# Kernel tuning notes

Hardware: AMD Instinct MI355X
Metric: run time of the kernel (lower is better)

## Reference

```python
import jax, jax.numpy as jnp
import numpy as np

N_NODES, N_EDGES = 8, 8
NODE_FEAT, EDGE_FEAT = 4, 3
NODE_EMB, EDGE_EMB = 9, 8
N_LAYER = 3
N_QUBITS = NODE_EMB + EDGE_EMB + 2  # 19

H_GATE = (jnp.array([[1, 1], [1, -1]], jnp.complex64) / np.sqrt(2).astype(np.float32))
CNOT4 = jnp.asarray(np.array([[1, 0, 0, 0], [0, 1, 0, 0], [0, 0, 0, 1], [0, 0, 1, 0]],
                             np.complex64).reshape(2, 2, 2, 2))


def rx_mat(t):
    c = jnp.cos(0.5 * t).astype(jnp.complex64)
    s = (-1j) * jnp.sin(0.5 * t).astype(jnp.complex64)
    return jnp.stack([jnp.stack([c, s]), jnp.stack([s, c])])


def rz_mat(t):
    e = jnp.exp(-0.5j * t.astype(jnp.complex64))
    z = jnp.zeros((), jnp.complex64)
    return jnp.stack([jnp.stack([e, z]), jnp.stack([z, jnp.conj(e)])])


def apply_1q(psi, U, w):
    psi = jnp.tensordot(U, psi, axes=((1,), (w,)))
    return jnp.moveaxis(psi, 0, w)


def apply_cnot(psi, c, t):
    psi = jnp.tensordot(CNOT4, psi, axes=((2, 3), (c, t)))
    return jnp.moveaxis(psi, (0, 1), (c, t))


def gcn_conv(x, src, dst, W, b, n):
    # PyG GCNConv: add self-loops, symmetric D^-1/2 (A+I) D^-1/2 normalization
    h = x @ W  # (n, out)
    src2 = jnp.concatenate([src, jnp.arange(n)])
    dst2 = jnp.concatenate([dst, jnp.arange(n)])
    deg = jax.ops.segment_sum(jnp.ones(src2.shape[0], x.dtype), dst2, num_segments=n)
    dis = jnp.where(deg > 0, jax.lax.rsqrt(jnp.maximum(deg, 1e-12)), 0.0)
    coef = dis[src2] * dis[dst2]
    out = jax.ops.segment_sum(h[src2] * coef[:, None], dst2, num_segments=n)
    return out + b


def quantum_circuit(feats, qweights):
    psi = jnp.zeros((2,) * N_QUBITS, jnp.complex64).at[(0,) * N_QUBITS].set(1.0)
    # feature_map: Hadamards + BasicEntanglerLayers(1 layer, rotation=RZ)
    for q in range(N_QUBITS):
        psi = apply_1q(psi, H_GATE, q)
    for q in range(N_QUBITS):
        psi = apply_1q(psi, rz_mat(feats[q]), q)
    for q in range(N_QUBITS):
        psi = apply_cnot(psi, q, (q + 1) % N_QUBITS)
    # two ansatz blocks (weights first dim is 2), each with N_LAYER layers
    for i in range(2):
        w = qweights[i]  # (N_QUBITS, N_LAYER)
        for j in range(N_LAYER):
            for q in range(N_QUBITS):
                psi = apply_1q(psi, rx_mat(w[q, j]), q)
                psi = apply_1q(psi, rz_mat(w[q, j]), q)
            for q in range(N_QUBITS):
                psi = apply_cnot(psi, q, (q + 1) % N_QUBITS)
    pr = jnp.sum(jnp.abs(psi.reshape(2, -1)) ** 2, axis=1)  # marginal of qubit 0
    return (pr[0] - pr[1]).astype(jnp.float32)  # <Z_0>


def setup_inputs() -> dict:
    key = jax.random.key(0)
    ks = jax.random.split(key, 20)
    inp = {
        "edge_index": jax.random.randint(ks[0], (2, N_EDGES), 0, N_NODES),
        "state": jax.random.normal(ks[1], (N_NODES, NODE_FEAT), jnp.float32),
        "mass": jax.random.normal(ks[2], (N_EDGES,), jnp.float32),
        "spin": jax.random.normal(ks[3], (N_EDGES,), jnp.float32),
        "charge": jax.random.normal(ks[4], (N_EDGES,), jnp.float32),
        "p_norm": jax.random.normal(ks[5], (1,), jnp.float32),
        "theta": jax.random.normal(ks[6], (1,), jnp.float32),
        "scattering": jax.random.normal(ks[7], (1,), jnp.float32),
        "gcn_node_w": jax.random.normal(ks[8], (NODE_FEAT, 1), jnp.float32) * 0.3,
        "gcn_node_b": jnp.zeros((1,), jnp.float32),
        "gcn_edge_w": jax.random.normal(ks[9], (EDGE_FEAT, 1), jnp.float32) * 0.3,
        "gcn_edge_b": jnp.zeros((1,), jnp.float32),
        "node_w": jax.random.normal(ks[10], (N_NODES, NODE_EMB), jnp.float32) * 0.3,
        "node_b": jnp.zeros((NODE_EMB,), jnp.float32),
        "edge_w": jax.random.normal(ks[11], (N_EDGES, EDGE_EMB), jnp.float32) * 0.3,
        "edge_b": jnp.zeros((EDGE_EMB,), jnp.float32),
        "qweights": jax.random.normal(ks[12], (2, N_QUBITS, N_LAYER), jnp.float32) * 0.1,
    }
    return inp


def reference(edge_index, state, mass, spin, charge, p_norm, theta, scattering,
              gcn_node_w, gcn_node_b, gcn_edge_w, gcn_edge_b,
              node_w, node_b, edge_w, edge_b, qweights):
    src, dst = edge_index[0], edge_index[1]
    x_edges = jnp.stack([mass, spin, charge], axis=1)  # (E, 3)
    x1 = gcn_conv(state, src, dst, gcn_node_w, gcn_node_b, N_NODES).reshape(-1)
    x1 = x1 @ node_w + node_b  # (NODE_EMB,)
    x2 = gcn_conv(x_edges, src, dst, gcn_edge_w, gcn_edge_b, N_EDGES).reshape(-1)
    x2 = x2 @ edge_w + edge_b  # (EDGE_EMB,)
    feats = jnp.concatenate([x1, x2, p_norm.reshape(-1), theta.reshape(-1)])  # (N_QUBITS,)
    return quantum_circuit(feats, qweights)
```

## Files before the change

### kernel.cpp

```cpp
#include <hip/hip_runtime.h>

#define NQ 19
#define SZ (1u << 19)

struct Params {
    const int* ei;
    const float* state; const float* mass; const float* spin; const float* charge;
    const float* p_norm; const float* theta;
    const float* gnw; const float* gnb; const float* gew; const float* geb;
    const float* nw; const float* nb; const float* ew; const float* eb;
    const float* qw;
    float2* buf0;
    unsigned* counter;
};

__device__ __forceinline__ unsigned pinv(unsigned c)
{
    unsigned y = (c ^ (c >> 1)) & 0x1FFFFu;
    unsigned c0 = c & 1u, c17 = (c >> 17) & 1u, c18 = (c >> 18) & 1u;
    return y | ((c0 ^ c17 ^ c18) << 17) | ((c0 ^ c18) << 18);
}

__device__ __forceinline__ unsigned padl(unsigned l) { return l + 2u * (l >> 3); }

__device__ __forceinline__ void bfly(float2& a, float2& b,
                                     float2 u00, float2 u01,
                                     float2 u10, float2 u11)
{
    float2 na, nb;
    na.x = u00.x * a.x - u00.y * a.y + u01.x * b.x - u01.y * b.y;
    na.y = u00.x * a.y + u00.y * a.x + u01.x * b.y + u01.y * b.x;
    nb.x = u10.x * a.x - u10.y * a.y + u11.x * b.x - u11.y * b.y;
    nb.y = u10.x * a.y + u10.y * a.x + u11.x * b.y + u11.y * b.x;
    a = na;
    b = nb;
}

__device__ __forceinline__ void apply_gates(float2 r[4], const float2* Gl,
                                            int ampbit0, int jbit0, int n)
{
    #pragma unroll
    for (int k = 0; k < n; ++k) {
        const float2 u00 = Gl[(ampbit0 + k) * 4 + 0];
        const float2 u01 = Gl[(ampbit0 + k) * 4 + 1];
        const float2 u10 = Gl[(ampbit0 + k) * 4 + 2];
        const float2 u11 = Gl[(ampbit0 + k) * 4 + 3];
        const int m = 1 << (jbit0 + k);
        #pragma unroll
        for (int j = 0; j < 4; ++j)
            if (!(j & m)) bfly(r[j], r[j | m], u00, u01, u10, u11);
    }
}

__device__ __forceinline__ void build_G(float2* shG, const float* qw, int layer,
                                        unsigned t)
{
    if (t < NQ) {
        int k = (int)t, q = 18 - k;
        double th = (double)qw[(layer / 3) * (NQ * 3) + q * 3 + (layer % 3)];
        double c = cos(0.5 * th), s = sin(0.5 * th);
        shG[k * 4 + 0] = make_float2((float)(c * c), (float)(-s * c));
        shG[k * 4 + 1] = make_float2((float)(-s * s), (float)(-c * s));
        shG[k * 4 + 2] = make_float2((float)(s * s), (float)(-c * s));
        shG[k * 4 + 3] = make_float2((float)(c * c), (float)(s * c));
    }
}

__device__ __forceinline__ void passA_tail(float2 r[4], const float2* Gl,
                                           unsigned t, float2* X0, float2* X1)
{
    apply_gates(r, Gl, 0, 0, 2);
    *reinterpret_cast<float4*>(&X0[padl(t << 2)]) =
        make_float4(r[0].x, r[0].y, r[1].x, r[1].y);
    *reinterpret_cast<float4*>(&X0[padl((t << 2) + 2u)]) =
        make_float4(r[2].x, r[2].y, r[3].x, r[3].y);
    __syncthreads();
    #pragma unroll
    for (int j = 0; j < 4; ++j)
        r[j] = X0[padl((t & 3u) | ((unsigned)j << 2) | ((t >> 2) << 4))];
    apply_gates(r, Gl, 2, 0, 2);
    #pragma unroll
    for (int j = 0; j < 4; ++j)
        X1[padl((t & 3u) | ((unsigned)j << 2) | ((t >> 2) << 4))] = r[j];
    __syncthreads();
    #pragma unroll
    for (int j = 0; j < 4; ++j)
        r[j] = X1[padl((t & 15u) | ((unsigned)j << 4) | ((t >> 4) << 6))];
    apply_gates(r, Gl, 4, 0, 2);
    #pragma unroll
    for (int j = 0; j < 4; ++j)
        X0[padl((t & 15u) | ((unsigned)j << 4) | ((t >> 4) << 6))] = r[j];
    __syncthreads();
    #pragma unroll
    for (int j = 0; j < 4; ++j)
        r[j] = X0[padl((t & 63u) | ((unsigned)j << 6) | ((t >> 6) << 8))];
    apply_gates(r, Gl, 6, 0, 2);
    #pragma unroll
    for (int j = 0; j < 4; ++j)
        X1[padl((t & 63u) | ((unsigned)j << 6) | ((t >> 6) << 8))] = r[j];
    __syncthreads();
    #pragma unroll
    for (int j = 0; j < 4; ++j)
        r[j] = X1[padl((t & 255u) | ((unsigned)j << 8) | ((t >> 8) << 10))];
    apply_gates(r, Gl, 8, 0, 2);
    #pragma unroll
    for (int j = 0; j < 4; ++j)
        X0[padl((t & 255u) | ((unsigned)j << 8) | ((t >> 8) << 10))] = r[j];
    __syncthreads();
    #pragma unroll
    for (int j = 0; j < 4; ++j)
        r[j] = X0[padl(t | ((unsigned)j << 9))];
    apply_gates(r, Gl, 10, 1, 1);
}

__device__ __forceinline__ void passB_gates(float2 r[4], const float2* Gl,
                                            unsigned t, float2* X0, float2* X1)
{
    apply_gates(r, Gl, 11, 0, 2);
    #pragma unroll
    for (int j = 0; j < 4; ++j)
        X0[padl((t & 7u) | ((unsigned)j << 3) | ((t >> 3) << 5))] = r[j];
    __syncthreads();
    #pragma unroll
    for (int j = 0; j < 4; ++j)
        r[j] = X0[padl((t & 31u) | ((unsigned)j << 5) | ((t >> 5) << 7))];
    apply_gates(r, Gl, 13, 0, 2);
    #pragma unroll
    for (int j = 0; j < 4; ++j)
        X1[padl((t & 31u) | ((unsigned)j << 5) | ((t >> 5) << 7))] = r[j];
    __syncthreads();
    #pragma unroll
    for (int j = 0; j < 4; ++j)
        r[j] = X1[padl((t & 127u) | ((unsigned)j << 7) | ((t >> 7) << 9))];
    apply_gates(r, Gl, 15, 0, 2);
    #pragma unroll
    for (int j = 0; j < 4; ++j)
        X0[padl((t & 127u) | ((unsigned)j << 7) | ((t >> 7) << 9))] = r[j];
    __syncthreads();
    #pragma unroll
    for (int j = 0; j < 4; ++j)
        r[j] = X0[padl(t | ((unsigned)j << 9))];
    apply_gates(r, Gl, 17, 0, 2);
}

__global__ __launch_bounds__(512, 4)
void k_A0(Params P)
{
    __shared__ __align__(16) float2 stage[5120];
    __shared__ __align__(16) float2 X0[2560];
    __shared__ float2 shG[NQ * 4];
    __shared__ double sh_feats[NQ];
    __shared__ double sh_S;

    const unsigned t = threadIdx.x;
    const unsigned blk = blockIdx.x;
    const unsigned base = blk << 11;

    if (blk == 0 && t == 0) *P.counter = 0u;

    if (t == 0) {
        double deg[8], dis[8], h[8], o1[8], he[8], o2[8];
        for (int v = 0; v < 8; ++v) deg[v] = 1.0;
        for (int e = 0; e < 8; ++e) deg[P.ei[8 + e]] += 1.0;
        for (int v = 0; v < 8; ++v) dis[v] = 1.0 / sqrt(deg[v]);
        for (int v = 0; v < 8; ++v) {
            double s = 0.0;
            for (int k = 0; k < 4; ++k)
                s += (double)P.state[v * 4 + k] * (double)P.gnw[k];
            h[v] = s;
        }
        for (int v = 0; v < 8; ++v) o1[v] = h[v] * dis[v] * dis[v] + (double)P.gnb[0];
        for (int e = 0; e < 8; ++e) {
            int s = P.ei[e], d = P.ei[8 + e];
            o1[d] += h[s] * dis[s] * dis[d];
        }
        for (int j = 0; j < 9; ++j) {
            double a = (double)P.nb[j];
            for (int v = 0; v < 8; ++v) a += o1[v] * (double)P.nw[v * 9 + j];
            sh_feats[j] = a;
        }
        for (int e = 0; e < 8; ++e)
            he[e] = (double)P.mass[e] * (double)P.gew[0]
                  + (double)P.spin[e] * (double)P.gew[1]
                  + (double)P.charge[e] * (double)P.gew[2];
        for (int v = 0; v < 8; ++v) o2[v] = he[v] * dis[v] * dis[v] + (double)P.geb[0];
        for (int e = 0; e < 8; ++e) {
            int s = P.ei[e], d = P.ei[8 + e];
            o2[d] += he[s] * dis[s] * dis[d];
        }
        for (int j = 0; j < 8; ++j) {
            double a = (double)P.eb[j];
            for (int v = 0; v < 8; ++v) a += o2[v] * (double)P.ew[v * 8 + j];
            sh_feats[9 + j] = a;
        }
        sh_feats[17] = (double)P.p_norm[0];
        sh_feats[18] = (double)P.theta[0];
        double S = 0.0;
        for (int q = 0; q < NQ; ++q) S += sh_feats[q];
        sh_S = S;
    }
    __syncthreads();

    build_G(shG, P.qw, 0, t);
    {
        double S = sh_S;
        for (unsigned m = t; m < 1024u; m += 512u) {
            double a = -0.5 * S;
            for (int k = 0; k < 10; ++k)
                if ((m >> k) & 1u) a += sh_feats[18 - k];
            double sp, cp;
            sincos(a, &sp, &cp);
            stage[m] = make_float2((float)cp, (float)sp);
        }
        const double amp = 1.0 / sqrt((double)SZ);
        for (unsigned m = t; m < 512u; m += 512u) {
            double a = 0.0;
            for (int k = 0; k < 9; ++k)
                if ((m >> k) & 1u) a += sh_feats[8 - k];
            double sp, cp;
            sincos(a, &sp, &cp);
            stage[1024u + m] = make_float2((float)(amp * cp), (float)(amp * sp));
        }
    }
    __syncthreads();

    float2 r[4];
    #pragma unroll
    for (int j = 0; j < 4; ++j) {
        unsigned li = (t << 2) | (unsigned)j;
        unsigned b = pinv(base | li);
        float2 e0 = stage[b & 1023u];
        float2 e1 = stage[1024u + (b >> 10)];
        r[j] = make_float2(e0.x * e1.x - e0.y * e1.y,
                           e0.x * e1.y + e0.y * e1.x);
    }
    passA_tail(r, shG, t, X0, stage);
    #pragma unroll
    for (int j = 0; j < 4; ++j)
        P.buf0[base | t | ((unsigned)j << 9)] = r[j];
}

__global__ __launch_bounds__(512, 4)
void k_A(const float2* __restrict__ in, float2* __restrict__ out,
         const float* __restrict__ qw, int layer)
{
    __shared__ __align__(16) float2 stage[5120];
    __shared__ __align__(16) float2 X0[2560];
    __shared__ float2 shG[NQ * 4];
    const unsigned t = threadIdx.x;
    const unsigned base = blockIdx.x << 11;

    build_G(shG, qw, layer, t);
    const unsigned R0 = pinv(base) & ~2047u;
    const unsigned R1 = pinv(base | 1u) & ~2047u;
    #pragma unroll
    for (int k = 0; k < 4; ++k) {
        unsigned i = ((unsigned)k << 10) | (t << 1);
        unsigned g = (i < 2048u) ? (R0 + i) : (R1 + (i - 2048u));
        *reinterpret_cast<float4*>(&stage[padl(i)]) =
            *reinterpret_cast<const float4*>(&in[g]);
    }
    __syncthreads();

    float2 r[4];
    #pragma unroll
    for (int j = 0; j < 4; ++j) {
        unsigned li = (t << 2) | (unsigned)j;
        unsigned b = pinv(base | li);
        r[j] = stage[padl(((li & 1u) << 11) | (b & 2047u))];
    }
    passA_tail(r, shG, t, X0, stage);
    #pragma unroll
    for (int j = 0; j < 4; ++j)
        out[base | t | ((unsigned)j << 9)] = r[j];
}

__global__ __launch_bounds__(512, 4)
void k_B(float2* __restrict__ buf, const float* __restrict__ qw, int layer,
         int do_reduce, double* __restrict__ partial,
         unsigned* __restrict__ counter, float* __restrict__ out)
{
    __shared__ __align__(16) float2 X0[2560];
    __shared__ __align__(16) float2 X1[2560];
    __shared__ double sm[512];
    __shared__ float2 shG[NQ * 4];
    __shared__ int who;
    const unsigned t = threadIdx.x;
    const unsigned blk = blockIdx.x;

    build_G(shG, qw, layer, t);
    float2 r[4];
    #pragma unroll
    for (int j = 0; j < 4; ++j) {
        unsigned li = (t & 7u) | ((unsigned)j << 3) | ((t >> 3) << 5);
        unsigned c = (li & 7u) | (blk << 3) | ((li >> 3) << 11);
        r[j] = buf[c];
    }
    __syncthreads();
    passB_gates(r, shG, t, X0, X1);

    if (do_reduce) {
        double acc = 0.0;
        #pragma unroll
        for (int j = 0; j < 4; ++j) {
            unsigned li = t | ((unsigned)j << 9);
            unsigned c = (li & 7u) | (blk << 3) | ((li >> 3) << 11);
            float2 v = r[j];
            double w = (double)v.x * v.x + (double)v.y * v.y;
            acc += (__popc(c & 0x3FFFFu) & 1) ? -w : w;
        }
        sm[t] = acc;
        __syncthreads();
        for (int st = 256; st > 0; st >>= 1) {
            if ((int)t < st) sm[t] += sm[t + st];
            __syncthreads();
        }
        if (t == 0) {
            partial[blk] = sm[0];
            __threadfence();
            unsigned old = atomicAdd(counter, 1u);
            who = (old == 255u);
        }
        __syncthreads();
        if (who) {
            double v = (t < 256u)
                ? __hip_atomic_load(&partial[t], __ATOMIC_RELAXED,
                                    __HIP_MEMORY_SCOPE_AGENT)
                : 0.0;
            sm[t] = v;
            __syncthreads();
            for (int st = 256; st > 0; st >>= 1) {
                if ((int)t < st) sm[t] += sm[t + st];
                __syncthreads();
            }
            if (t == 0) out[0] = (float)sm[0];
        }
    } else {
        #pragma unroll
        for (int j = 0; j < 4; ++j) {
            unsigned li = t | ((unsigned)j << 9);
            unsigned c = (li & 7u) | (blk << 3) | ((li >> 3) << 11);
            buf[c] = r[j];
        }
    }
}

extern "C" void kernel_launch(void* const* d_in, const int* in_sizes, int n_in,
                              void* d_out, int out_size, void* d_ws, size_t ws_size,
                              hipStream_t stream)
{
    char* ws = (char*)d_ws;
    double*   partial = (double*)(ws + 16384);
    unsigned* counter = (unsigned*)(ws + 20480);
    float2*   buf0    = (float2*)(ws + 32768);
    float2*   buf1    = buf0 + SZ;
    const float* qw   = (const float*)d_in[16];
    float* out        = (float*)d_out;

    Params P;
    P.ei      = (const int*)d_in[0];
    P.state   = (const float*)d_in[1];
    P.mass    = (const float*)d_in[2];
    P.spin    = (const float*)d_in[3];
    P.charge  = (const float*)d_in[4];
    P.p_norm  = (const float*)d_in[5];
    P.theta   = (const float*)d_in[6];
    P.gnw     = (const float*)d_in[8];
    P.gnb     = (const float*)d_in[9];
    P.gew     = (const float*)d_in[10];
    P.geb     = (const float*)d_in[11];
    P.nw      = (const float*)d_in[12];
    P.nb      = (const float*)d_in[13];
    P.ew      = (const float*)d_in[14];
    P.eb      = (const float*)d_in[15];
    P.qw      = qw;
    P.buf0    = buf0;
    P.counter = counter;

    k_A0<<<256, 512, 0, stream>>>(P);
    k_B<<<256, 512, 0, stream>>>(buf0, qw, 0, 0, partial, counter, out);
    for (int l = 1; l <= 5; ++l) {
        float2* in  = (l & 1) ? buf0 : buf1;
        float2* o   = (l & 1) ? buf1 : buf0;
        k_A<<<256, 512, 0, stream>>>(in, o, qw, l);
        k_B<<<256, 512, 0, stream>>>(o, qw, l, l == 5, partial, counter, out);
    }
}
```

Measured before the change: 104.1 us.

## Apply in-block gates via wavefront shuffles instead of shared-memory transposes

Rewrites the per-block gate passes so that most amplitude-bit gates are applied across lanes with 64-wide xor shuffles, instead of through repeated shared-memory transposes with a barrier each. Pass A drops from five LDS round-trips to one, and pass B from three to one. It also removes the second LDS buffer in k_B and issues global loads before building the gate table so the two overlap. The cost is extra ALU work for select-based butterflies and shuffle latency, and a new thread-to-index mapping that must stay correct.

```diff
diff --git a/kernel.cpp b/kernel.cpp
--- a/kernel.cpp
+++ b/kernel.cpp
@@ -52,6 +52,30 @@
     }
 }
 
+__device__ __forceinline__ void shfl_gate(float2 r[4], const float2* Gl,
+                                          int ampbit, int lanebit)
+{
+    const float2 u00 = Gl[ampbit * 4 + 0], u01 = Gl[ampbit * 4 + 1];
+    const float2 u10 = Gl[ampbit * 4 + 2], u11 = Gl[ampbit * 4 + 3];
+    const int side = (threadIdx.x >> lanebit) & 1;
+    const float2 u0 = side ? u10 : u00;
+    const float2 u1 = side ? u11 : u01;
+    #pragma unroll
+    for (int j = 0; j < 4; ++j) {
+        double d;
+        __builtin_memcpy(&d, &r[j], 8);
+        d = __shfl_xor(d, 1 << lanebit, 64);
+        float2 p;
+        __builtin_memcpy(&p, &d, 8);
+        float2 a = side ? p : r[j];
+        float2 b = side ? r[j] : p;
+        float2 n;
+        n.x = u0.x * a.x - u0.y * a.y + u1.x * b.x - u1.y * b.y;
+        n.y = u0.x * a.y + u0.y * a.x + u1.x * b.y + u1.y * b.x;
+        r[j] = n;
+    }
+}
+
 __device__ __forceinline__ void build_G(float2* shG, const float* qw, int layer,
                                         unsigned t)
 {
@@ -66,81 +90,52 @@
     }
 }
 
-__device__ __forceinline__ void passA_tail(float2 r[4], const float2* Gl,
-                                           unsigned t, float2* X0, float2* X1)
-{
-    apply_gates(r, Gl, 0, 0, 2);
-    *reinterpret_cast<float4*>(&X0[padl(t << 2)]) =
-        make_float4(r[0].x, r[0].y, r[1].x, r[1].y);
-    *reinterpret_cast<float4*>(&X0[padl((t << 2) + 2u)]) =
-        make_float4(r[2].x, r[2].y, r[3].x, r[3].y);
-    __syncthreads();
-    #pragma unroll
-    for (int j = 0; j < 4; ++j)
-        r[j] = X0[padl((t & 3u) | ((unsigned)j << 2) | ((t >> 2) << 4))];
-    apply_gates(r, Gl, 2, 0, 2);
-    #pragma unroll
-    for (int j = 0; j < 4; ++j)
-        X1[padl((t & 3u) | ((unsigned)j << 2) | ((t >> 2) << 4))] = r[j];
-    __syncthreads();
-    #pragma unroll
-    for (int j = 0; j < 4; ++j)
-        r[j] = X1[padl((t & 15u) | ((unsigned)j << 4) | ((t >> 4) << 6))];
-    apply_gates(r, Gl, 4, 0, 2);
-    #pragma unroll
-    for (int j = 0; j < 4; ++j)
-        X0[padl((t & 15u) | ((unsigned)j << 4) | ((t >> 4) << 6))] = r[j];
-    __syncthreads();
-    #pragma unroll
-    for (int j = 0; j < 4; ++j)
-        r[j] = X0[padl((t & 63u) | ((unsigned)j << 6) | ((t >> 6) << 8))];
-    apply_gates(r, Gl, 6, 0, 2);
-    #pragma unroll
-    for (int j = 0; j < 4; ++j)
-        X1[padl((t & 63u) | ((unsigned)j << 6) | ((t >> 6) << 8))] = r[j];
-    __syncthreads();
-    #pragma unroll
-    for (int j = 0; j < 4; ++j)
-        r[j] = X1[padl((t & 255u) | ((unsigned)j << 8) | ((t >> 8) << 10))];
-    apply_gates(r, Gl, 8, 0, 2);
-    #pragma unroll
-    for (int j = 0; j < 4; ++j)
-        X0[padl((t & 255u) | ((unsigned)j << 8) | ((t >> 8) << 10))] = r[j];
-    __syncthreads();
-    #pragma unroll
-    for (int j = 0; j < 4; ++j)
-        r[j] = X0[padl(t | ((unsigned)j << 9))];
-    apply_gates(r, Gl, 10, 1, 1);
-}
-
-__device__ __forceinline__ void passB_gates(float2 r[4], const float2* Gl,
-                                            unsigned t, float2* X0, float2* X1)
-{
-    apply_gates(r, Gl, 11, 0, 2);
-    #pragma unroll
-    for (int j = 0; j < 4; ++j)
-        X0[padl((t & 7u) | ((unsigned)j << 3) | ((t >> 3) << 5))] = r[j];
-    __syncthreads();
-    #pragma unroll
-    for (int j = 0; j < 4; ++j)
-        r[j] = X0[padl((t & 31u) | ((unsigned)j << 5) | ((t >> 5) << 7))];
-    apply_gates(r, Gl, 13, 0, 2);
-    #pragma unroll
-    for (int j = 0; j < 4; ++j)
-        X1[padl((t & 31u) | ((unsigned)j << 5) | ((t >> 5) << 7))] = r[j];
-    __syncthreads();
-    #pragma unroll
-    for (int j = 0; j < 4; ++j)
-        r[j] = X1[padl((t & 127u) | ((unsigned)j << 7) | ((t >> 7) << 9))];
-    apply_gates(r, Gl, 15, 0, 2);
-    #pragma unroll
-    for (int j = 0; j < 4; ++j)
-        X0[padl((t & 127u) | ((unsigned)j << 7) | ((t >> 7) << 9))] = r[j];
-    __syncthreads();
-    #pragma unroll
-    for (int j = 0; j < 4; ++j)
-        r[j] = X0[padl(t | ((unsigned)j << 9))];
-    apply_gates(r, Gl, 17, 0, 2);
+__device__ __forceinline__ unsigned liA1(unsigned lam, unsigned hi, unsigned j)
+{
+    return j | ((lam & 31u) << 2) | ((lam >> 5) << 8)
+             | ((hi & 1u) << 7) | ((hi >> 1) << 9);
+}
+__device__ __forceinline__ unsigned liA2(unsigned lam, unsigned hi, unsigned j)
+{
+    return (lam & 31u) | ((lam >> 5) << 7) | ((hi & 3u) << 5)
+         | ((hi >> 2) << 8) | (j << 9);
+}
+__device__ __forceinline__ void passA_tail(float2 r[4], const float2* shG,
+                                           unsigned lam, unsigned hi, float2* X0)
+{
+    apply_gates(r, shG, 0, 0, 2);
+    shfl_gate(r, shG, 2, 0);
+    shfl_gate(r, shG, 3, 1);
+    shfl_gate(r, shG, 4, 2);
+    shfl_gate(r, shG, 5, 3);
+    shfl_gate(r, shG, 6, 4);
+    shfl_gate(r, shG, 8, 5);
+    {
+        unsigned lb = liA1(lam, hi, 0);
+        *reinterpret_cast<float4*>(&X0[padl(lb)]) =
+            make_float4(r[0].x, r[0].y, r[1].x, r[1].y);
+        *reinterpret_cast<float4*>(&X0[padl(lb + 2u)]) =
+            make_float4(r[2].x, r[2].y, r[3].x, r[3].y);
+    }
+    __syncthreads();
+    #pragma unroll
+    for (int j = 0; j < 4; ++j)
+        r[j] = X0[padl(liA2(lam, hi, (unsigned)j))];
+    shfl_gate(r, shG, 7, 5);
+    apply_gates(r, shG, 9, 0, 2);
+}
+
+__device__ __forceinline__ unsigned liB1(unsigned lam, unsigned hi, unsigned j)
+{
+    return (lam & 7u) | (j << 3) | (((lam >> 3) & 7u) << 5) | (hi << 8);
+}
+__device__ __forceinline__ unsigned liB2(unsigned lam, unsigned hi, unsigned j)
+{
+    return (lam & 31u) | ((lam >> 5) << 8) | ((hi & 7u) << 5) | (j << 9);
+}
+__device__ __forceinline__ unsigned cB(unsigned li, unsigned blk)
+{
+    return (li & 7u) | (blk << 3) | ((li >> 3) << 11);
 }
 
 __global__ __launch_bounds__(512, 4)
@@ -153,6 +148,7 @@
     __shared__ double sh_S;
 
     const unsigned t = threadIdx.x;
+    const unsigned lam = t & 63u, hi = t >> 6;
     const unsigned blk = blockIdx.x;
     const unsigned base = blk << 11;
 
@@ -227,17 +223,17 @@
     float2 r[4];
     #pragma unroll
     for (int j = 0; j < 4; ++j) {
-        unsigned li = (t << 2) | (unsigned)j;
+        unsigned li = liA1(lam, hi, (unsigned)j);
         unsigned b = pinv(base | li);
         float2 e0 = stage[b & 1023u];
         float2 e1 = stage[1024u + (b >> 10)];
         r[j] = make_float2(e0.x * e1.x - e0.y * e1.y,
                            e0.x * e1.y + e0.y * e1.x);
     }
-    passA_tail(r, shG, t, X0, stage);
-    #pragma unroll
-    for (int j = 0; j < 4; ++j)
-        P.buf0[base | t | ((unsigned)j << 9)] = r[j];
+    passA_tail(r, shG, lam, hi, X0);
+    #pragma unroll
+    for (int j = 0; j < 4; ++j)
+        P.buf0[base | liA2(lam, hi, (unsigned)j)] = r[j];
 }
 
 __global__ __launch_bounds__(512, 4)
@@ -248,31 +244,37 @@
     __shared__ __align__(16) float2 X0[2560];
     __shared__ float2 shG[NQ * 4];
     const unsigned t = threadIdx.x;
+    const unsigned lam = t & 63u, hi = t >> 6;
     const unsigned base = blockIdx.x << 11;
 
-    build_G(shG, qw, layer, t);
     const unsigned R0 = pinv(base) & ~2047u;
     const unsigned R1 = pinv(base | 1u) & ~2047u;
+    float4 v[4];
     #pragma unroll
     for (int k = 0; k < 4; ++k) {
         unsigned i = ((unsigned)k << 10) | (t << 1);
         unsigned g = (i < 2048u) ? (R0 + i) : (R1 + (i - 2048u));
-        *reinterpret_cast<float4*>(&stage[padl(i)]) =
-            *reinterpret_cast<const float4*>(&in[g]);
+        v[k] = *reinterpret_cast<const float4*>(&in[g]);
+    }
+    build_G(shG, qw, layer, t);
+    #pragma unroll
+    for (int k = 0; k < 4; ++k) {
+        unsigned i = ((unsigned)k << 10) | (t << 1);
+        *reinterpret_cast<float4*>(&stage[padl(i)]) = v[k];
     }
     __syncthreads();
 
     float2 r[4];
     #pragma unroll
     for (int j = 0; j < 4; ++j) {
-        unsigned li = (t << 2) | (unsigned)j;
+        unsigned li = liA1(lam, hi, (unsigned)j);
         unsigned b = pinv(base | li);
         r[j] = stage[padl(((li & 1u) << 11) | (b & 2047u))];
     }
-    passA_tail(r, shG, t, X0, stage);
-    #pragma unroll
-    for (int j = 0; j < 4; ++j)
-        out[base | t | ((unsigned)j << 9)] = r[j];
+    passA_tail(r, shG, lam, hi, X0);
+    #pragma unroll
+    for (int j = 0; j < 4; ++j)
+        out[base | liA2(lam, hi, (unsigned)j)] = r[j];
 }
 
 __global__ __launch_bounds__(512, 4)
@@ -281,30 +283,39 @@
          unsigned* __restrict__ counter, float* __restrict__ out)
 {
     __shared__ __align__(16) float2 X0[2560];
-    __shared__ __align__(16) float2 X1[2560];
     __shared__ double sm[512];
     __shared__ float2 shG[NQ * 4];
     __shared__ int who;
     const unsigned t = threadIdx.x;
+    const unsigned lam = t & 63u, hi = t >> 6;
     const unsigned blk = blockIdx.x;
 
+    float2 r[4];
+    #pragma unroll
+    for (int j = 0; j < 4; ++j)
+        r[j] = buf[cB(liB1(lam, hi, (unsigned)j), blk)];
     build_G(shG, qw, layer, t);
-    float2 r[4];
-    #pragma unroll
-    for (int j = 0; j < 4; ++j) {
-        unsigned li = (t & 7u) | ((unsigned)j << 3) | ((t >> 3) << 5);
-        unsigned c = (li & 7u) | (blk << 3) | ((li >> 3) << 11);
-        r[j] = buf[c];
-    }
-    __syncthreads();
-    passB_gates(r, shG, t, X0, X1);
+    __syncthreads();
+
+    apply_gates(r, shG, 11, 0, 2);
+    shfl_gate(r, shG, 13, 3);
+    shfl_gate(r, shG, 14, 4);
+    shfl_gate(r, shG, 15, 5);
+    #pragma unroll
+    for (int j = 0; j < 4; ++j)
+        X0[padl(liB1(lam, hi, (unsigned)j))] = r[j];
+    __syncthreads();
+    #pragma unroll
+    for (int j = 0; j < 4; ++j)
+        r[j] = X0[padl(liB2(lam, hi, (unsigned)j))];
+    shfl_gate(r, shG, 16, 5);
+    apply_gates(r, shG, 17, 0, 2);
 
     if (do_reduce) {
         double acc = 0.0;
         #pragma unroll
         for (int j = 0; j < 4; ++j) {
-            unsigned li = t | ((unsigned)j << 9);
-            unsigned c = (li & 7u) | (blk << 3) | ((li >> 3) << 11);
+            unsigned c = cB(liB2(lam, hi, (unsigned)j), blk);
             float2 v = r[j];
             double w = (double)v.x * v.x + (double)v.y * v.y;
             acc += (__popc(c & 0x3FFFFu) & 1) ? -w : w;
@@ -337,11 +348,8 @@
         }
     } else {
         #pragma unroll
-        for (int j = 0; j < 4; ++j) {
-            unsigned li = t | ((unsigned)j << 9);
-            unsigned c = (li & 7u) | (blk << 3) | ((li >> 3) << 11);
-            buf[c] = r[j];
-        }
+        for (int j = 0; j < 4; ++j)
+            buf[cB(liB2(lam, hi, (unsigned)j), blk)] = r[j];
     }
 }
 
```

Result: slower. 110.5 us (+6.1%).
